# Performance work log

Hardware: AMD Instinct MI355X
Metric: run time of the kernel (lower is better)

## Reference

```python
import jax, jax.numpy as jnp
import numpy as np

TAG_THR = 0.1
MIN_HEIGHT = 0.0
PULL_WEIGHT = 1.0
PUSH_WEIGHT = 1.0
EPS = 1e-6


def _bbox_iou(boxes):
    # boxes: [N,4] -> IoU [N,N] (standard, no +1 offset; heights in the loss
    # are also computed without +1)
    x1, y1, x2, y2 = boxes[:, 0], boxes[:, 1], boxes[:, 2], boxes[:, 3]
    area = (x2 - x1) * (y2 - y1)
    iw = jnp.clip(jnp.minimum(x2[:, None], x2[None, :]) - jnp.maximum(x1[:, None], x1[None, :]), 0.0)
    ih = jnp.clip(jnp.minimum(y2[:, None], y2[None, :]) - jnp.maximum(y1[:, None], y1[None, :]), 0.0)
    inter = iw * ih
    union = area[:, None] + area[None, :] - inter
    return inter / jnp.maximum(union, 1e-12)


def _single_image(pred, gt_inds, proposals):
    # pred [N,D], gt_inds [N] int, proposals [N,5]
    N = pred.shape[0]
    heights = proposals[:, 3] - proposals[:, 1]
    valid = (gt_inds >= 0) & (heights > MIN_HEIGHT)
    scores = proposals[:, 4]
    iou = _bbox_iou(proposals[:, :4])  # [N,N]

    def step(state, _):
        alive, tot_pull, tot_push, pull_cnt, push_cnt = state
        active = jnp.sum(alive) >= 2  # pop i; if nothing remains, the torch loop breaks
        # i = highest-scoring remaining proposal (greedy, score-sorted)
        i = jnp.argmax(jnp.where(alive, scores, -jnp.inf))
        rem = alive.at[i].set(False)
        overlap = (iou[i] > 0.0) & rem
        diff = jnp.mean((pred - pred[i]) ** 2, axis=1)  # [N]
        check = diff < TAG_THR
        same = gt_inds == gt_inds[i]
        pull_m = overlap & same & ~check
        push_m = overlap & ~same & check
        pn = jnp.sum(pull_m)
        qn = jnp.sum(push_m)
        pull_l = jnp.sum(jnp.where(pull_m, diff * scores, 0.0)) / jnp.maximum(pn, 1).astype(diff.dtype)
        push_l = jnp.sum(jnp.where(push_m, jnp.exp(-diff) * scores, 0.0)) / jnp.maximum(qn, 1).astype(diff.dtype)
        add_pull = active & (pn > 0)
        add_push = active & (qn > 0)
        tot_pull = tot_pull + jnp.where(add_pull, pull_l, 0.0)
        tot_push = tot_push + jnp.where(add_push, push_l, 0.0)
        pull_cnt = pull_cnt + add_pull.astype(jnp.float32)
        push_cnt = push_cnt + add_push.astype(jnp.float32)
        # suppress everything overlapping i whose tag is already close (diff < thr)
        new_alive = rem & ~(overlap & check)
        alive = jnp.where(active, new_alive, alive)
        return (alive, tot_pull, tot_push, pull_cnt, push_cnt), None

    z = jnp.float32(0.0)
    init = (valid, z, z, z, z)
    (_, tot_pull, tot_push, pull_cnt, push_cnt), _ = jax.lax.scan(step, init, None, length=N)
    pull = tot_pull / (pull_cnt + EPS)
    push = tot_push / (push_cnt + EPS)
    return push, pull


def setup_inputs() -> dict:
    key = jax.random.key(0)
    k1, k2, k3, k4, k5, k6, k7 = jax.random.split(key, 7)
    IMGS, N, D = 4, 2000, 4
    pred = jax.random.normal(k1, (IMGS, N, D), dtype=jnp.float32)
    gt_inds = jax.random.randint(k2, (IMGS, N), 0, 50, dtype=jnp.int32)
    x1 = jax.random.uniform(k3, (IMGS, N), minval=0.0, maxval=800.0)
    y1 = jax.random.uniform(k4, (IMGS, N), minval=0.0, maxval=800.0)
    w = jax.random.uniform(k5, (IMGS, N), minval=8.0, maxval=128.0)
    h = jax.random.uniform(k6, (IMGS, N), minval=8.0, maxval=128.0)
    score = jax.random.uniform(k7, (IMGS, N), minval=0.0, maxval=1.0)
    proposals = jnp.stack([x1, y1, x1 + w, y1 + h, score], axis=-1).astype(jnp.float32)
    gt_bboxes = jax.random.uniform(jax.random.fold_in(key, 9), (IMGS, 20, 4), dtype=jnp.float32)
    return {"pred": pred, "gt_inds": gt_inds, "proposals": proposals, "gt_bboxes": gt_bboxes}


def reference(pred, gt_inds, proposals, gt_bboxes):
    # gt_bboxes is accepted by the torch forward but never used in the loss math.
    push, pull = jax.vmap(_single_image)(pred, gt_inds, proposals)  # per-image scalars
    img_num = pred.shape[0]
    push_loss = jnp.sum(push) / img_num * PUSH_WEIGHT
    pull_loss = jnp.sum(pull) / img_num * PULL_WEIGHT
    return push_loss, pull_loss
```

## Files before the change

### kernel.cpp

```cpp
#include <hip/hip_runtime.h>
#include <stdint.h>

#define BLOCK 256
#define KMAX 8
#define NWAVES (BLOCK / 64)
#define S2 2048
#define NW 32
#define NCH 32
#define SPB 16
#define PB (S2 / SPB)
#define RB (S2 / BLOCK)
#define EFF_INF 0x7FFFFFFF

__device__ inline int rank_of(const unsigned long long* ss, int j) {
    int jw = j >> 6, jb = j & 63;
    int rk = __popcll(ss[jw] & (jb ? (~0ull >> (64 - jb)) : 0ull));
    for (int w = 0; w < jw; ++w) rk += __popcll(ss[w]);
    return rk;
}

__global__ __launch_bounds__(BLOCK) void rankcount_kernel(
    const float* __restrict__ proposals,
    int* __restrict__ partial, int N, int imgs)
{
    const int bi = blockIdx.x, bj = blockIdx.y, img = blockIdx.z;
    const int t = threadIdx.x;
    const float* P = proposals + (size_t)img * N * 5;
    __shared__ unsigned sj[BLOCK];
    const int jbase = bj * BLOCK;
    {
        int j = jbase + t;
        sj[t] = (j < N) ? __float_as_uint(P[j*5 + 4]) : 0u;
    }
    __syncthreads();
    const int i = bi * BLOCK + t;
    if (i >= N) return;
    const unsigned my = __float_as_uint(P[i*5 + 4]);
    int p = 0;
    const uint4* s4 = (const uint4*)sj;
#pragma unroll
    for (int q = 0; q < BLOCK/4; ++q) {
        uint4 v = s4[q];
        int jj = jbase + q*4;
        p += (int)((v.x > my) | ((v.x == my) & (jj + 0 < i)));
        p += (int)((v.y > my) | ((v.y == my) & (jj + 1 < i)));
        p += (int)((v.z > my) | ((v.z == my) & (jj + 2 < i)));
        p += (int)((v.w > my) | ((v.w == my) & (jj + 3 < i)));
    }
    partial[((size_t)(img*RB + bj))*S2 + i] = p;
}

__global__ __launch_bounds__(BLOCK) void rankscatter_kernel(
    const float* __restrict__ pred, const int* __restrict__ gt_inds,
    const float* __restrict__ proposals, const int* __restrict__ partial,
    float* __restrict__ soa, int* __restrict__ sgt, int N, int imgs)
{
    const int img = blockIdx.y, t = threadIdx.x;
    const int i = blockIdx.x * BLOCK + t;
    const size_t stride = (size_t)imgs * S2;
    const size_t base   = (size_t)img * S2;

    if (i >= N) {
        if (i < S2) {
#pragma unroll
            for (int a = 0; a < 9; ++a) soa[(size_t)a*stride + base + i] = 0.f;
            sgt[base + i] = -1;
        }
        return;
    }

    const float* P = proposals + (size_t)img * N * 5;
    const float* E = pred      + (size_t)img * N * 4;
    const int*   G = gt_inds   + (size_t)img * N;

    const float p0 = P[i*5+0], p1 = P[i*5+1], p2 = P[i*5+2],
                p3 = P[i*5+3], p4 = P[i*5+4];
    const float q0 = E[i*4+0], q1 = E[i*4+1], q2 = E[i*4+2], q3 = E[i*4+3];
    const int   gg = G[i];

    int p = 0;
#pragma unroll
    for (int b = 0; b < RB; ++b)
        p += partial[((size_t)(img*RB + b))*S2 + i];

    soa[0*stride + base + p] = p0;
    soa[1*stride + base + p] = p1;
    soa[2*stride + base + p] = p2;
    soa[3*stride + base + p] = p3;
    soa[4*stride + base + p] = p4;
    soa[5*stride + base + p] = q0;
    soa[6*stride + base + p] = q1;
    soa[7*stride + base + p] = q2;
    soa[8*stride + base + p] = q3;
    sgt[base + p] = gg;
}

__global__ __launch_bounds__(BLOCK) void supmat_kernel(
    const float* __restrict__ soa, unsigned long long* __restrict__ supT,
    int N, int imgs)
{
    const int ic = blockIdx.x, jc = blockIdx.y, img = blockIdx.z;
    if (ic < jc) return;
    const int t = threadIdx.x, wave = t >> 6, lane = t & 63;
    const size_t stride = (size_t)imgs * S2, base = (size_t)img * S2;
    __shared__ float si[8][64];
    for (int idx = t; idx < 512; idx += BLOCK) {
        int f = idx >> 6, e = idx & 63;
        int a = (f < 4) ? f : f + 1;
        si[f][e] = soa[(size_t)a*stride + base + ic*64 + e];
    }
    __syncthreads();
    const int j = jc*64 + lane;
    const float jx1 = soa[0*stride+base+j], jy1 = soa[1*stride+base+j];
    const float jx2 = soa[2*stride+base+j], jy2 = soa[3*stride+base+j];
    const float j0  = soa[5*stride+base+j], j1  = soa[6*stride+base+j];
    const float j2  = soa[7*stride+base+j], j3  = soa[8*stride+base+j];
    const bool jin = (j < N);
    for (int ii = 0; ii < 16; ++ii) {
        int il = wave*16 + ii;
        int i  = ic*64 + il;
        float bx1 = si[0][il], by1 = si[1][il], bx2 = si[2][il], by2 = si[3][il];
        float f0  = si[4][il], f1  = si[5][il], f2  = si[6][il], f3  = si[7][il];
        bool s = false;
        if (jin && i < N) {
            float iw = fminf(jx2, bx2) - fmaxf(jx1, bx1);
            float ih = fminf(jy2, by2) - fmaxf(jy1, by1);
            if (iw > 0.f && ih > 0.f) {
                float d0 = j0-f0, d1 = j1-f1, d2 = j2-f2, d3 = j3-f3;
                float diff = 0.25f*(d0*d0 + d1*d1 + d2*d2 + d3*d3);
                s = diff < 0.1f;
            }
        }
        unsigned long long bb = __ballot(s);
        if (lane == 0)
            supT[((size_t)img*NCH + ic)*(NW*64) + (size_t)jc*64 + il] = bb;
    }
}

typedef __attribute__((address_space(1))) void* gas_vp;
typedef __attribute__((address_space(3))) void* las_vp;

#define SBW 2048
#define LCNT(c) (((c) + 2) / 2)

#define GR_PRE(c)                                                              \
    {                                                                          \
        const unsigned long long* blk = MB + ((size_t)(c))*(NW*64);            \
        _Pragma("unroll")                                                      \
        for (int k = 0; k < LCNT(c); ++k) {                                    \
            __builtin_amdgcn_global_load_lds(                                  \
                (gas_vp)(blk + k*128 + l*2),                                   \
                (las_vp)(sbuf + ((c)%3)*SBW + k*128), 16, 0, 0);               \
        }                                                                      \
    }

#define GR_STEP(c)                                                             \
    {                                                                          \
        if ((c) + 2 < NCH) GR_PRE((c)+2)                                       \
        asm volatile("s_waitcnt vmcnt(%0)" :: "i"(                             \
            ((c)+2 < NCH) ? (LCNT((c)+1) + LCNT((c)+2)) :                      \
            (((c)+1 < NCH) ? LCNT((c)+1) : 0)) : "memory");                    \
        const unsigned long long* cb = sbuf + ((c)%3)*SBW;                     \
        unsigned long long acc = 0ull;                                         \
        _Pragma("unroll")                                                      \
        for (int w = 0; w < (c); ++w) acc |= cb[w*64 + l] & sselA[w];          \
        const unsigned long long loc = cb[(c)*64 + l];                         \
        bool alive = ((vmask >> (c)) & 1u) && (acc == 0ull);                   \
        unsigned long long U = __ballot(alive);                                \
        unsigned long long sel = 0ull;                                         \
        while (U) {                                                            \
            bool inU = (U >> l) & 1ull;                                        \
            unsigned long long A = __ballot(inU && ((loc & U & lowmask) == 0ull)); \
            sel |= A;                                                          \
            bool kill = inU && !((A >> l) & 1ull) && ((loc & A) != 0ull);      \
            unsigned long long K = __ballot(kill);                             \
            U &= ~(A | K);                                                     \
        }                                                                      \
        if (l == 0) sselA[(c)] = sel;                                          \
    }

__global__ __launch_bounds__(64) void greedy_kernel(
    const unsigned long long* __restrict__ supT,
    const int* __restrict__ sgt, const float* __restrict__ soa,
    unsigned long long* __restrict__ selw_out, int imgs)
{
    const int img = blockIdx.x, l = threadIdx.x;
    const size_t stride = (size_t)imgs * S2, base = (size_t)img * S2;
    const unsigned long long* MB = supT + (size_t)img * NCH * (NW*64);
    __shared__ __attribute__((aligned(16))) unsigned long long sbuf[3 * SBW];
    __shared__ unsigned long long sselA[NW];

    unsigned vmask = 0u;
#pragma unroll
    for (int c = 0; c < NCH; ++c) {
        const int j = c*64 + l;
        int g = sgt[base + j];
        float a = soa[1*stride + base + j];
        float b = soa[3*stride + base + j];
        if (g >= 0 && (b - a) > 0.f) vmask |= (1u << c);
    }

    const unsigned long long lowmask = (l == 0) ? 0ull : (~0ull >> (64 - l));

    GR_PRE(0) GR_PRE(1)
    GR_STEP(0)  GR_STEP(1)  GR_STEP(2)  GR_STEP(3)
    GR_STEP(4)  GR_STEP(5)  GR_STEP(6)  GR_STEP(7)
    GR_STEP(8)  GR_STEP(9)  GR_STEP(10) GR_STEP(11)
    GR_STEP(12) GR_STEP(13) GR_STEP(14) GR_STEP(15)
    GR_STEP(16) GR_STEP(17) GR_STEP(18) GR_STEP(19)
    GR_STEP(20) GR_STEP(21) GR_STEP(22) GR_STEP(23)
    GR_STEP(24) GR_STEP(25) GR_STEP(26) GR_STEP(27)
    GR_STEP(28) GR_STEP(29) GR_STEP(30) GR_STEP(31)

    if (l < NW) selw_out[(size_t)img*NW + l] = sselA[l];
}

__global__ __launch_bounds__(BLOCK) void effsteps_kernel(
    const unsigned long long* __restrict__ supT,
    const unsigned long long* __restrict__ selw,
    const int* __restrict__ sgt, const float* __restrict__ soa,
    int* __restrict__ eff, int* __restrict__ nsteps, int imgs)
{
    const int img = blockIdx.x, t = threadIdx.x;
    const int lane = t & 63, wave = t >> 6;
    const size_t stride = (size_t)imgs * S2, base = (size_t)img * S2;
    const unsigned long long* M = supT + (size_t)img * NW * S2;
    __shared__ unsigned long long ss[NW];
    __shared__ unsigned hist[S2];
    __shared__ int ints[2*NWAVES];
    __shared__ unsigned wsum[NWAVES];
    __shared__ int bm[NWAVES];
    if (t < NW) ss[t] = selw[(size_t)img*NW + t];
    for (int x = t; x < S2; x += BLOCK) hist[x] = 0u;
    __syncthreads();

    int myV = 0, mySc = 0;
#pragma unroll
    for (int k = 0; k < 8; ++k) {
        const int j = k*BLOCK + t;
        const int jw_ = j >> 6;
        int g = sgt[base + j];
        float a = soa[1*stride+base+j], b = soa[3*stride+base+j];
        bool valid = (g >= 0) && ((b - a) > 0.f);
        bool selb  = (ss[jw_] >> (j & 63)) & 1ull;
        int e;
        if (!valid) e = 0;
        else if (selb) { e = rank_of(ss, j); ++myV; ++mySc; }
        else {
            ++myV;
            int istar = -1;
#pragma unroll
            for (int w = 0; w < NW; ++w) {
                if (w <= jw_) {
                    unsigned long long f = M[((size_t)jw_*NW + w)*64 + (j & 63)] & ss[w];
                    if (istar < 0 && f) istar = w*64 + __builtin_ctzll(f);
                }
            }
            if (istar < 0) e = EFF_INF;
            else { e = rank_of(ss, istar) + 1; atomicAdd(&hist[e - 1], 1u); }
        }
        eff[(size_t)img*S2 + j] = e;
    }
    __syncthreads();

    int v = myV, sc = mySc;
    for (int o = 32; o > 0; o >>= 1) { v += __shfl_down(v, o); sc += __shfl_down(sc, o); }
    if (lane == 0) { ints[wave] = v; ints[NWAVES + wave] = sc; }
    __syncthreads();
    int V = 0, Sc = 0;
    for (int w = 0; w < NWAVES; ++w) { V += ints[w]; Sc += ints[NWAVES + w]; }

    unsigned loc[8]; unsigned s = 0;
#pragma unroll
    for (int k = 0; k < 8; ++k) { s += hist[t*8 + k]; loc[k] = s; }
    unsigned tot = s;
    for (int o = 1; o < 64; o <<= 1) {
        unsigned u = __shfl_up(tot, o);
        if (lane >= o) tot += u;
    }
    if (lane == 63) wsum[wave] = tot;
    __syncthreads();
    unsigned woff = 0;
    for (int w = 0; w < wave; ++w) woff += wsum[w];
    unsigned exclP = woff + tot - s;
    __syncthreads();
#pragma unroll
    for (int k = 0; k < 8; ++k) hist[t*8 + k] = exclP + loc[k];
    __syncthreads();

    int best = EFF_INF;
    for (int r = t; r < Sc; r += BLOCK) {
        unsigned rem = (r == 0) ? 0u : hist[r - 1];
        int alive = V - r - (int)rem;
        if (alive < 2) best = min(best, r);
    }
    for (int o = 32; o > 0; o >>= 1) best = min(best, __shfl_down(best, o));
    if (lane == 0) bm[wave] = best;
    __syncthreads();
    if (t == 0) {
        int b = bm[0];
        for (int w = 1; w < NWAVES; ++w) b = min(b, bm[w]);
        nsteps[img] = min(b, Sc);
    }
}

__global__ __launch_bounds__(BLOCK) void pairs_kernel(
    const float* __restrict__ soa, const int* __restrict__ sgt,
    const int* __restrict__ eff, const unsigned long long* __restrict__ selw,
    const int* __restrict__ nsteps, float* __restrict__ partials, int imgs)
{
    const int ic = blockIdx.x, img = blockIdx.y;
    const int t = threadIdx.x, wave = t >> 6, lane = t & 63;
    const size_t stride = (size_t)imgs * S2, base = (size_t)img * S2;
    __shared__ unsigned long long ss[NW];
    __shared__ float pw[NWAVES][4];
    __shared__ int anyact;
    if (t < NW) ss[t] = selw[(size_t)img*NW + t];
    if (t == 0) anyact = 0;
    __syncthreads();
    const int ns = nsteps[img];

    float bx1[4], by1[4], bx2[4], by2[4], f0[4], f1[4], f2[4], f3[4];
    int bgt[4], rk[4]; bool act[4];
    bool any = false;
#pragma unroll
    for (int u = 0; u < 4; ++u) {
        const int i = ic*SPB + wave*4 + u;
        bool selb = (ss[i>>6] >> (i & 63)) & 1ull;
        int r = rank_of(ss, i);
        rk[u] = r;
        act[u] = selb && (r < ns);
        any |= act[u];
        if (act[u]) {
            bx1[u] = soa[0*stride+base+i]; by1[u] = soa[1*stride+base+i];
            bx2[u] = soa[2*stride+base+i]; by2[u] = soa[3*stride+base+i];
            f0[u]  = soa[5*stride+base+i]; f1[u]  = soa[6*stride+base+i];
            f2[u]  = soa[7*stride+base+i]; f3[u]  = soa[8*stride+base+i];
            bgt[u] = sgt[base + i];
        } else {
            bx1[u]=by1[u]=bx2[u]=by2[u]=0.f; f0[u]=f1[u]=f2[u]=f3[u]=0.f; bgt[u]=-2;
        }
    }
    if (any && lane == 0) anyact = 1;
    __syncthreads();
    if (!anyact) {
        if (t < 4) partials[((size_t)img*PB + ic)*4 + t] = 0.f;
        return;
    }

    float ps[4] = {0,0,0,0}, pn[4] = {0,0,0,0}, qs[4] = {0,0,0,0}, qn[4] = {0,0,0,0};
    for (int jt = 0; jt < NCH; ++jt) {
        const int j = jt*64 + lane;
        const float jx1 = soa[0*stride+base+j], jy1 = soa[1*stride+base+j];
        const float jx2 = soa[2*stride+base+j], jy2 = soa[3*stride+base+j];
        const float jsc = soa[4*stride+base+j];
        const float j0  = soa[5*stride+base+j], j1  = soa[6*stride+base+j];
        const float j2  = soa[7*stride+base+j], j3  = soa[8*stride+base+j];
        const int   jgt = sgt[base + j];
        const int   jef = eff[(size_t)img*S2 + j];
#pragma unroll
        for (int u = 0; u < 4; ++u) {
            if (!act[u]) continue;
            if (rk[u] < jef) {
                float iw = fminf(jx2, bx2[u]) - fmaxf(jx1, bx1[u]);
                float ih = fminf(jy2, by2[u]) - fmaxf(jy1, by1[u]);
                if (iw > 0.f && ih > 0.f) {
                    float d0 = j0 - f0[u], d1 = j1 - f1[u];
                    float d2 = j2 - f2[u], d3 = j3 - f3[u];
                    float diff = 0.25f*(d0*d0 + d1*d1 + d2*d2 + d3*d3);
                    bool check = diff < 0.1f;
                    bool same  = (jgt == bgt[u]);
                    if (same && !check)      { ps[u] += diff * jsc;       pn[u] += 1.f; }
                    else if (!same && check) { qs[u] += expf(-diff)*jsc;  qn[u] += 1.f; }
                }
            }
        }
    }

    float sPull = 0.f, cPull = 0.f, sPush = 0.f, cPush = 0.f;
#pragma unroll
    for (int u = 0; u < 4; ++u) {
        if (!act[u]) continue;
        float a0 = ps[u], a1 = pn[u], a2 = qs[u], a3 = qn[u];
        for (int o = 32; o > 0; o >>= 1) {
            a0 += __shfl_down(a0, o); a1 += __shfl_down(a1, o);
            a2 += __shfl_down(a2, o); a3 += __shfl_down(a3, o);
        }
        if (lane == 0) {
            if (a1 > 0.f) { sPull += a0 / a1; cPull += 1.f; }
            if (a3 > 0.f) { sPush += a2 / a3; cPush += 1.f; }
        }
    }
    if (lane == 0) {
        pw[wave][0] = sPull; pw[wave][1] = cPull;
        pw[wave][2] = sPush; pw[wave][3] = cPush;
    }
    __syncthreads();
    if (t == 0) {
        float a = 0, b = 0, c = 0, d = 0;
        for (int w = 0; w < NWAVES; ++w) {
            a += pw[w][0]; b += pw[w][1]; c += pw[w][2]; d += pw[w][3];
        }
        float* p = partials + ((size_t)img*PB + ic)*4;
        p[0] = a; p[1] = b; p[2] = c; p[3] = d;
    }
}

__global__ __launch_bounds__(BLOCK) void finalize_kernel(
    const float* __restrict__ partials, float* __restrict__ out, int imgs)
{
    const int t = threadIdx.x;
    __shared__ float a[8][4];
    if (t < 32) ((float*)a)[t] = 0.f;
    __syncthreads();
    for (int e = t; e < imgs * PB; e += BLOCK) {
        int img = e / PB;
        const float* p = partials + (size_t)e * 4;
#pragma unroll
        for (int k = 0; k < 4; ++k) {
            float v = p[k];
            if (v != 0.f) atomicAdd(&a[img][k], v);
        }
    }
    __syncthreads();
    if (t == 0) {
        float push = 0.f, pull = 0.f;
        for (int i = 0; i < imgs; ++i) {
            pull += a[i][0] / (a[i][1] + 1e-6f);
            push += a[i][2] / (a[i][3] + 1e-6f);
        }
        out[0] = push / (float)imgs;
        out[1] = pull / (float)imgs;
    }
}

__global__ __launch_bounds__(BLOCK) void tagloss_kernel(
    const float* __restrict__ pred, const int* __restrict__ gt_inds,
    const float* __restrict__ proposals, float* __restrict__ ws, int N)
{
    const int img = blockIdx.x, t = threadIdx.x;
    const int lane = t & 63, wav = t >> 6;
    const float* P = proposals + (size_t)img * N * 5;
    const float* E = pred      + (size_t)img * N * 4;
    const int*   G = gt_inds   + (size_t)img * N;
    float x1[KMAX], y1[KMAX], x2[KMAX], y2[KMAX], sc[KMAX];
    float e0[KMAX], e1[KMAX], e2[KMAX], e3[KMAX];
    int gt[KMAX]; unsigned amask = 0u; int local_alive = 0;
#pragma unroll
    for (int k = 0; k < KMAX; ++k) {
        int j = k * BLOCK + t;
        if (j < N) {
            x1[k]=P[j*5+0]; y1[k]=P[j*5+1]; x2[k]=P[j*5+2]; y2[k]=P[j*5+3]; sc[k]=P[j*5+4];
            e0[k]=E[j*4+0]; e1[k]=E[j*4+1]; e2[k]=E[j*4+2]; e3[k]=E[j*4+3]; gt[k]=G[j];
            if (gt[k] >= 0 && (y2[k]-y1[k]) > 0.0f) { amask |= 1u<<k; local_alive++; }
        } else { x1[k]=y1[k]=x2[k]=y2[k]=0.f; sc[k]=0.f; e0[k]=e1[k]=e2[k]=e3[k]=0.f; gt[k]=-1; }
    }
    __shared__ unsigned long long s_key[NWAVES];
    __shared__ float s_b[9];
    __shared__ float s_part[NWAVES][5];
    int alive_count;
    {
        float v = (float)local_alive;
#pragma unroll
        for (int o = 32; o > 0; o >>= 1) v += __shfl_down(v, o);
        if (lane == 0) s_part[wav][0] = v;
        __syncthreads();
        float tot = 0.f;
        for (int w = 0; w < NWAVES; ++w) tot += s_part[w][0];
        alive_count = (int)tot;
    }
    float tot_pull=0.f, tot_push=0.f, pull_cnt=0.f, push_cnt=0.f;
    while (alive_count >= 2) {
        unsigned long long key = 0ull;
#pragma unroll
        for (int k = 0; k < KMAX; ++k)
            if (amask & (1u<<k)) {
                unsigned long long kk = ((unsigned long long)__float_as_uint(sc[k])<<32)
                                      | (unsigned long long)(0xFFFFFFFFu - (unsigned)(k*BLOCK+t));
                if (kk > key) key = kk;
            }
#pragma unroll
        for (int o = 32; o > 0; o >>= 1) {
            unsigned long long ok = __shfl_down(key, o);
            if (ok > key) key = ok;
        }
        if (lane == 0) s_key[wav] = key;
        __syncthreads();
        unsigned long long bk = s_key[0];
        for (int w = 1; w < NWAVES; ++w) if (s_key[w] > bk) bk = s_key[w];
        const int i = (int)(0xFFFFFFFFu - (unsigned)(bk & 0xFFFFFFFFull));
        if ((i & (BLOCK-1)) == t) {
            int k = i / BLOCK;
            s_b[0]=x1[k]; s_b[1]=y1[k]; s_b[2]=x2[k]; s_b[3]=y2[k];
            s_b[4]=e0[k]; s_b[5]=e1[k]; s_b[6]=e2[k]; s_b[7]=e3[k];
            s_b[8]=__int_as_float(gt[k]);
        }
        __syncthreads();
        const float bx1=s_b[0], by1=s_b[1], bx2=s_b[2], by2=s_b[3];
        const float f0=s_b[4], f1=s_b[5], f2=s_b[6], f3=s_b[7];
        const int bgt = __float_as_int(s_b[8]);
        const float areai = (bx2-bx1)*(by2-by1);
        float psum=0.f,qsum=0.f,pn=0.f,qn=0.f,scnt=0.f;
#pragma unroll
        for (int k = 0; k < KMAX; ++k) {
            if (!(amask & (1u<<k))) continue;
            int j = k*BLOCK+t;
            if (j == i) { amask &= ~(1u<<k); continue; }
            float iw = fmaxf(fminf(x2[k],bx2)-fmaxf(x1[k],bx1),0.f);
            float ih = fmaxf(fminf(y2[k],by2)-fmaxf(y1[k],by1),0.f);
            float inter = iw*ih;
            float uni = (x2[k]-x1[k])*(y2[k]-y1[k]) + areai - inter;
            float iou = inter / fmaxf(uni, 1e-12f);
            if (iou > 0.f) {
                float d0=e0[k]-f0,d1=e1[k]-f1,d2=e2[k]-f2,d3=e3[k]-f3;
                float diff = 0.25f*(d0*d0+d1*d1+d2*d2+d3*d3);
                bool check = diff < 0.1f;
                bool same = (gt[k]==bgt);
                if (same && !check) { psum += diff*sc[k]; pn += 1.f; }
                if (!same && check) { qsum += __expf(-diff)*sc[k]; qn += 1.f; }
                if (check)          { amask &= ~(1u<<k); scnt += 1.f; }
            }
        }
        float r0=psum,r1=pn,r2=qsum,r3=qn,r4=scnt;
#pragma unroll
        for (int o = 32; o > 0; o >>= 1) {
            r0+=__shfl_down(r0,o); r1+=__shfl_down(r1,o); r2+=__shfl_down(r2,o);
            r3+=__shfl_down(r3,o); r4+=__shfl_down(r4,o);
        }
        if (lane == 0) { s_part[wav][0]=r0;s_part[wav][1]=r1;s_part[wav][2]=r2;s_part[wav][3]=r3;s_part[wav][4]=r4; }
        __syncthreads();
        float T0=0,T1=0,T2=0,T3=0,T4=0;
        for (int w = 0; w < NWAVES; ++w) {
            T0+=s_part[w][0];T1+=s_part[w][1];T2+=s_part[w][2];T3+=s_part[w][3];T4+=s_part[w][4];
        }
        if (T1 > 0.f) { tot_pull += T0/T1; pull_cnt += 1.f; }
        if (T3 > 0.f) { tot_push += T2/T3; push_cnt += 1.f; }
        alive_count -= 1 + (int)T4;
    }
    if (t == 0) {
        ws[img*2+0] = tot_push / (push_cnt + 1e-6f);
        ws[img*2+1] = tot_pull / (pull_cnt + 1e-6f);
    }
}

__global__ void finalize_fb_kernel(const float* __restrict__ ws,
                                   float* __restrict__ out, int imgs)
{
    if (threadIdx.x == 0 && blockIdx.x == 0) {
        float push = 0.f, pull = 0.f;
        for (int k = 0; k < imgs; ++k) { push += ws[2*k]; pull += ws[2*k+1]; }
        out[0] = push / (float)imgs;
        out[1] = pull / (float)imgs;
    }
}

extern "C" void kernel_launch(void* const* d_in, const int* in_sizes, int n_in,
                              void* d_out, int out_size, void* d_ws, size_t ws_size,
                              hipStream_t stream) {
    const float* pred      = (const float*)d_in[0];
    const int*   gt_inds   = (const int*)  d_in[1];
    const float* proposals = (const float*)d_in[2];
    const int imgs = in_sizes[3] / 80;
    const int N    = in_sizes[1] / imgs;

    size_t off = 0;
    auto alloc = [&](size_t b) { size_t o = off; off += (b + 255) & ~(size_t)255; return o; };
    const size_t soa_off  = alloc((size_t)9 * imgs * S2 * 4);
    const size_t sgt_off  = alloc((size_t)imgs * S2 * 4);
    const size_t sel_off  = alloc((size_t)imgs * NW * 8);
    const size_t eff_off  = alloc((size_t)imgs * S2 * 4);
    const size_t sup_off  = alloc((size_t)imgs * S2 * NW * 8);
    const size_t nst_off  = alloc((size_t)imgs * 4);
    const size_t par_off  = alloc((size_t)imgs * PB * 16);
    const size_t rnk_off  = alloc((size_t)imgs * RB * S2 * 4);
    const size_t need = off;

    if (N <= S2 && imgs <= 8 && ws_size >= need) {
        char* w = (char*)d_ws;
        float*              soa  = (float*)(w + soa_off);
        int*                sgt  = (int*)(w + sgt_off);
        unsigned long long* sel  = (unsigned long long*)(w + sel_off);
        int*                eff  = (int*)(w + eff_off);
        unsigned long long* supT = (unsigned long long*)(w + sup_off);
        int*                nst  = (int*)(w + nst_off);
        float*              par  = (float*)(w + par_off);
        int*                rnk  = (int*)(w + rnk_off);

        rankcount_kernel<<<dim3(RB, RB, imgs), BLOCK, 0, stream>>>(
            proposals, rnk, N, imgs);
        rankscatter_kernel<<<dim3(RB, imgs), BLOCK, 0, stream>>>(
            pred, gt_inds, proposals, rnk, soa, sgt, N, imgs);
        supmat_kernel<<<dim3(NCH, NCH, imgs), BLOCK, 0, stream>>>(soa, supT, N, imgs);
        greedy_kernel<<<imgs, 64, 0, stream>>>(supT, sgt, soa, sel, imgs);
        effsteps_kernel<<<imgs, BLOCK, 0, stream>>>(supT, sel, sgt, soa, eff, nst, imgs);
        pairs_kernel<<<dim3(PB, imgs), BLOCK, 0, stream>>>(soa, sgt, eff, sel,
                                                           nst, par, imgs);
        finalize_kernel<<<1, BLOCK, 0, stream>>>(par, (float*)d_out, imgs);
    } else {
        float* ws = (float*)d_ws;
        tagloss_kernel<<<imgs, BLOCK, 0, stream>>>(pred, gt_inds, proposals, ws, N);
        finalize_fb_kernel<<<1, 64, 0, stream>>>(ws, (float*)d_out, imgs);
    }
}
```

Baseline: 172.0 us.

## Replace dense suppression bitmatrix with compacted sparse pair list

The suppression relation is now stored as an atomically compacted list of (j,i) pairs instead of a dense per-image 2048x2048 bit matrix. The greedy kernel rebuilds each 64-wide diagonal block from the list in LDS and propagates kills forward. The effsteps kernel finds the first selected suppressor with an atomicMin over the pairs. This avoids writing and reading the dense matrix, at the cost of repeatedly scanning the pair list on every one of the 32 chunk steps in a single-wave kernel. A fixed capacity (PCAP) silently truncates pairs if the count overflows.

```diff
diff --git a/kernel.cpp b/kernel.cpp
--- a/kernel.cpp
+++ b/kernel.cpp
@@ -10,6 +10,8 @@
 #define SPB 16
 #define PB (S2 / SPB)
 #define RB (S2 / BLOCK)
+#define PCAP 65536
+#define LDSP 6144
 #define EFF_INF 0x7FFFFFFF
 
 __device__ inline int rank_of(const unsigned long long* ss, int j) {
@@ -21,10 +23,11 @@
 
 __global__ __launch_bounds__(BLOCK) void rankcount_kernel(
     const float* __restrict__ proposals,
-    int* __restrict__ partial, int N, int imgs)
+    int* __restrict__ partial, int* __restrict__ pcnt, int N, int imgs)
 {
     const int bi = blockIdx.x, bj = blockIdx.y, img = blockIdx.z;
     const int t = threadIdx.x;
+    if (bi == 0 && bj == 0 && t == 0) pcnt[img] = 0;
     const float* P = proposals + (size_t)img * N * 5;
     __shared__ unsigned sj[BLOCK];
     const int jbase = bj * BLOCK;
@@ -95,9 +98,9 @@
     sgt[base + p] = gg;
 }
 
-__global__ __launch_bounds__(BLOCK) void supmat_kernel(
-    const float* __restrict__ soa, unsigned long long* __restrict__ supT,
-    int N, int imgs)
+__global__ __launch_bounds__(BLOCK) void suppairs_kernel(
+    const float* __restrict__ soa, unsigned* __restrict__ pairs,
+    int* __restrict__ pcnt, int N, int imgs)
 {
     const int ic = blockIdx.x, jc = blockIdx.y, img = blockIdx.z;
     if (ic < jc) return;
@@ -116,13 +119,14 @@
     const float j0  = soa[5*stride+base+j], j1  = soa[6*stride+base+j];
     const float j2  = soa[7*stride+base+j], j3  = soa[8*stride+base+j];
     const bool jin = (j < N);
+    unsigned* PL = pairs + (size_t)img * PCAP;
     for (int ii = 0; ii < 16; ++ii) {
         int il = wave*16 + ii;
         int i  = ic*64 + il;
         float bx1 = si[0][il], by1 = si[1][il], bx2 = si[2][il], by2 = si[3][il];
         float f0  = si[4][il], f1  = si[5][il], f2  = si[6][il], f3  = si[7][il];
         bool s = false;
-        if (jin && i < N) {
+        if (jin && i < N && i > j) {
             float iw = fminf(jx2, bx2) - fmaxf(jx1, bx1);
             float ih = fminf(jy2, by2) - fmaxf(jy1, by1);
             if (iw > 0.f && ih > 0.f) {
@@ -131,92 +135,85 @@
                 s = diff < 0.1f;
             }
         }
-        unsigned long long bb = __ballot(s);
-        if (lane == 0)
-            supT[((size_t)img*NCH + ic)*(NW*64) + (size_t)jc*64 + il] = bb;
-    }
-}
-
-typedef __attribute__((address_space(1))) void* gas_vp;
-typedef __attribute__((address_space(3))) void* las_vp;
-
-#define SBW 2048
-#define LCNT(c) (((c) + 2) / 2)
-
-#define GR_PRE(c)                                                              \
-    {                                                                          \
-        const unsigned long long* blk = MB + ((size_t)(c))*(NW*64);            \
-        _Pragma("unroll")                                                      \
-        for (int k = 0; k < LCNT(c); ++k) {                                    \
-            __builtin_amdgcn_global_load_lds(                                  \
-                (gas_vp)(blk + k*128 + l*2),                                   \
-                (las_vp)(sbuf + ((c)%3)*SBW + k*128), 16, 0, 0);               \
-        }                                                                      \
-    }
-
-#define GR_STEP(c)                                                             \
-    {                                                                          \
-        if ((c) + 2 < NCH) GR_PRE((c)+2)                                       \
-        asm volatile("s_waitcnt vmcnt(%0)" :: "i"(                             \
-            ((c)+2 < NCH) ? (LCNT((c)+1) + LCNT((c)+2)) :                      \
-            (((c)+1 < NCH) ? LCNT((c)+1) : 0)) : "memory");                    \
-        const unsigned long long* cb = sbuf + ((c)%3)*SBW;                     \
-        unsigned long long acc = 0ull;                                         \
-        _Pragma("unroll")                                                      \
-        for (int w = 0; w < (c); ++w) acc |= cb[w*64 + l] & sselA[w];          \
-        const unsigned long long loc = cb[(c)*64 + l];                         \
-        bool alive = ((vmask >> (c)) & 1u) && (acc == 0ull);                   \
-        unsigned long long U = __ballot(alive);                                \
-        unsigned long long sel = 0ull;                                         \
-        while (U) {                                                            \
-            bool inU = (U >> l) & 1ull;                                        \
-            unsigned long long A = __ballot(inU && ((loc & U & lowmask) == 0ull)); \
-            sel |= A;                                                          \
-            bool kill = inU && !((A >> l) & 1ull) && ((loc & A) != 0ull);      \
-            unsigned long long K = __ballot(kill);                             \
-            U &= ~(A | K);                                                     \
-        }                                                                      \
-        if (l == 0) sselA[(c)] = sel;                                          \
-    }
+        unsigned long long m = __ballot(s);
+        if (m) {
+            int leader = __ffsll((unsigned long long)m) - 1;
+            int basei = 0;
+            if (lane == leader) basei = atomicAdd(&pcnt[img], __popcll(m));
+            basei = __shfl(basei, leader);
+            if (s) {
+                int idx = basei + __popcll(m & ((lane == 0) ? 0ull : (~0ull >> (64 - lane))));
+                if (idx < PCAP) PL[idx] = ((unsigned)j << 11) | (unsigned)i;
+            }
+        }
+    }
+}
 
 __global__ __launch_bounds__(64) void greedy_kernel(
-    const unsigned long long* __restrict__ supT,
+    const unsigned* __restrict__ pairs, const int* __restrict__ pcnt,
     const int* __restrict__ sgt, const float* __restrict__ soa,
     unsigned long long* __restrict__ selw_out, int imgs)
 {
     const int img = blockIdx.x, l = threadIdx.x;
     const size_t stride = (size_t)imgs * S2, base = (size_t)img * S2;
-    const unsigned long long* MB = supT + (size_t)img * NCH * (NW*64);
-    __shared__ __attribute__((aligned(16))) unsigned long long sbuf[3 * SBW];
-    __shared__ unsigned long long sselA[NW];
-
-    unsigned vmask = 0u;
-#pragma unroll
+    __shared__ unsigned long long skilled[NW], ssel[NW], sloc[64];
+    __shared__ unsigned spair[LDSP];
+
+    int P = pcnt[img]; if (P > PCAP) P = PCAP;
+    const unsigned* PL = pairs + (size_t)img * PCAP;
+    const bool staged = (P <= LDSP);
+    if (staged) for (int p = l; p < P; p += 64) spair[p] = PL[p];
+
     for (int c = 0; c < NCH; ++c) {
         const int j = c*64 + l;
         int g = sgt[base + j];
         float a = soa[1*stride + base + j];
         float b = soa[3*stride + base + j];
-        if (g >= 0 && (b - a) > 0.f) vmask |= (1u << c);
-    }
+        bool invalid = !(g >= 0 && (b - a) > 0.f);
+        unsigned long long bb = __ballot(invalid);
+        if (l == 0) skilled[c] = bb;
+    }
+    __syncthreads();
 
     const unsigned long long lowmask = (l == 0) ? 0ull : (~0ull >> (64 - l));
 
-    GR_PRE(0) GR_PRE(1)
-    GR_STEP(0)  GR_STEP(1)  GR_STEP(2)  GR_STEP(3)
-    GR_STEP(4)  GR_STEP(5)  GR_STEP(6)  GR_STEP(7)
-    GR_STEP(8)  GR_STEP(9)  GR_STEP(10) GR_STEP(11)
-    GR_STEP(12) GR_STEP(13) GR_STEP(14) GR_STEP(15)
-    GR_STEP(16) GR_STEP(17) GR_STEP(18) GR_STEP(19)
-    GR_STEP(20) GR_STEP(21) GR_STEP(22) GR_STEP(23)
-    GR_STEP(24) GR_STEP(25) GR_STEP(26) GR_STEP(27)
-    GR_STEP(28) GR_STEP(29) GR_STEP(30) GR_STEP(31)
-
-    if (l < NW) selw_out[(size_t)img*NW + l] = sselA[l];
+    for (int c = 0; c < NCH; ++c) {
+        sloc[l] = 0ull;
+        __syncthreads();
+        for (int p = l; p < P; p += 64) {
+            unsigned v = staged ? spair[p] : PL[p];
+            int lo = v >> 11, hi = v & 2047;
+            if ((lo >> 6) == c && (hi >> 6) == c)
+                atomicOr(&sloc[hi & 63], 1ull << (lo & 63));
+        }
+        __syncthreads();
+        unsigned long long U = ~skilled[c];
+        const unsigned long long loc = sloc[l];
+        unsigned long long sel = 0ull;
+        while (U) {
+            bool inU = (U >> l) & 1ull;
+            unsigned long long A = __ballot(inU && ((loc & U & lowmask) == 0ull));
+            sel |= A;
+            bool kill = inU && !((A >> l) & 1ull) && ((loc & A) != 0ull);
+            unsigned long long K = __ballot(kill);
+            U &= ~(A | K);
+        }
+        if (l == 0) ssel[c] = sel;
+        if (sel != 0ull) {
+            for (int p = l; p < P; p += 64) {
+                unsigned v = staged ? spair[p] : PL[p];
+                int lo = v >> 11, hi = v & 2047;
+                if ((lo >> 6) == c && ((sel >> (lo & 63)) & 1ull) && (hi >> 6) > c)
+                    atomicOr(&skilled[hi >> 6], 1ull << (hi & 63));
+            }
+        }
+        __syncthreads();
+    }
+    if (l < NW) selw_out[(size_t)img*NW + l] = ssel[l];
 }
 
 __global__ __launch_bounds__(BLOCK) void effsteps_kernel(
-    const unsigned long long* __restrict__ supT,
+    const unsigned* __restrict__ pairs, const int* __restrict__ pcnt,
     const unsigned long long* __restrict__ selw,
     const int* __restrict__ sgt, const float* __restrict__ soa,
     int* __restrict__ eff, int* __restrict__ nsteps, int imgs)
@@ -224,39 +221,40 @@
     const int img = blockIdx.x, t = threadIdx.x;
     const int lane = t & 63, wave = t >> 6;
     const size_t stride = (size_t)imgs * S2, base = (size_t)img * S2;
-    const unsigned long long* M = supT + (size_t)img * NW * S2;
     __shared__ unsigned long long ss[NW];
+    __shared__ int sistar[S2];
     __shared__ unsigned hist[S2];
     __shared__ int ints[2*NWAVES];
     __shared__ unsigned wsum[NWAVES];
     __shared__ int bm[NWAVES];
     if (t < NW) ss[t] = selw[(size_t)img*NW + t];
-    for (int x = t; x < S2; x += BLOCK) hist[x] = 0u;
+    for (int x = t; x < S2; x += BLOCK) { sistar[x] = EFF_INF; hist[x] = 0u; }
+    __syncthreads();
+
+    int P = pcnt[img]; if (P > PCAP) P = PCAP;
+    const unsigned* PL = pairs + (size_t)img * PCAP;
+    for (int p = t; p < P; p += BLOCK) {
+        unsigned v = PL[p];
+        int lo = v >> 11, hi = v & 2047;
+        if ((ss[lo >> 6] >> (lo & 63)) & 1ull) atomicMin(&sistar[hi], lo);
+    }
     __syncthreads();
 
     int myV = 0, mySc = 0;
 #pragma unroll
     for (int k = 0; k < 8; ++k) {
         const int j = k*BLOCK + t;
-        const int jw_ = j >> 6;
         int g = sgt[base + j];
         float a = soa[1*stride+base+j], b = soa[3*stride+base+j];
         bool valid = (g >= 0) && ((b - a) > 0.f);
-        bool selb  = (ss[jw_] >> (j & 63)) & 1ull;
+        bool selb  = (ss[j>>6] >> (j & 63)) & 1ull;
         int e;
         if (!valid) e = 0;
         else if (selb) { e = rank_of(ss, j); ++myV; ++mySc; }
         else {
             ++myV;
-            int istar = -1;
-#pragma unroll
-            for (int w = 0; w < NW; ++w) {
-                if (w <= jw_) {
-                    unsigned long long f = M[((size_t)jw_*NW + w)*64 + (j & 63)] & ss[w];
-                    if (istar < 0 && f) istar = w*64 + __builtin_ctzll(f);
-                }
-            }
-            if (istar < 0) e = EFF_INF;
+            int istar = sistar[j];
+            if (istar == EFF_INF) e = EFF_INF;
             else { e = rank_of(ss, istar) + 1; atomicAdd(&hist[e - 1], 1u); }
         }
         eff[(size_t)img*S2 + j] = e;
@@ -569,10 +567,11 @@
     const size_t sgt_off  = alloc((size_t)imgs * S2 * 4);
     const size_t sel_off  = alloc((size_t)imgs * NW * 8);
     const size_t eff_off  = alloc((size_t)imgs * S2 * 4);
-    const size_t sup_off  = alloc((size_t)imgs * S2 * NW * 8);
     const size_t nst_off  = alloc((size_t)imgs * 4);
     const size_t par_off  = alloc((size_t)imgs * PB * 16);
     const size_t rnk_off  = alloc((size_t)imgs * RB * S2 * 4);
+    const size_t prs_off  = alloc((size_t)imgs * PCAP * 4);
+    const size_t pcn_off  = alloc((size_t)imgs * 4);
     const size_t need = off;
 
     if (N <= S2 && imgs <= 8 && ws_size >= need) {
@@ -581,18 +580,21 @@
         int*                sgt  = (int*)(w + sgt_off);
         unsigned long long* sel  = (unsigned long long*)(w + sel_off);
         int*                eff  = (int*)(w + eff_off);
-        unsigned long long* supT = (unsigned long long*)(w + sup_off);
         int*                nst  = (int*)(w + nst_off);
         float*              par  = (float*)(w + par_off);
         int*                rnk  = (int*)(w + rnk_off);
+        unsigned*           prs  = (unsigned*)(w + prs_off);
+        int*                pcn  = (int*)(w + pcn_off);
 
         rankcount_kernel<<<dim3(RB, RB, imgs), BLOCK, 0, stream>>>(
-            proposals, rnk, N, imgs);
+            proposals, rnk, pcn, N, imgs);
         rankscatter_kernel<<<dim3(RB, imgs), BLOCK, 0, stream>>>(
             pred, gt_inds, proposals, rnk, soa, sgt, N, imgs);
-        supmat_kernel<<<dim3(NCH, NCH, imgs), BLOCK, 0, stream>>>(soa, supT, N, imgs);
-        greedy_kernel<<<imgs, 64, 0, stream>>>(supT, sgt, soa, sel, imgs);
-        effsteps_kernel<<<imgs, BLOCK, 0, stream>>>(supT, sel, sgt, soa, eff, nst, imgs);
+        suppairs_kernel<<<dim3(NCH, NCH, imgs), BLOCK, 0, stream>>>(
+            soa, prs, pcn, N, imgs);
+        greedy_kernel<<<imgs, 64, 0, stream>>>(prs, pcn, sgt, soa, sel, imgs);
+        effsteps_kernel<<<imgs, BLOCK, 0, stream>>>(prs, pcn, sel, sgt, soa,
+                                                    eff, nst, imgs);
         pairs_kernel<<<dim3(PB, imgs), BLOCK, 0, stream>>>(soa, sgt, eff, sel,
                                                            nst, par, imgs);
         finalize_kernel<<<1, BLOCK, 0, stream>>>(par, (float*)d_out, imgs);
```

New measurement: 175.1 us. No clear change (+1.8%).
